# Optimization experiments

Measured on AMD Instinct MI355X. Metric: run time of the kernel, lower is better.

The kernel has to match this reference:

```python
import jax, jax.numpy as jnp
import numpy as np

D_MODEL = 1024
NUM_HEADS = 16
DEPTH = D_MODEL // NUM_HEADS
B, S = 2, 2048


def setup_inputs() -> dict:
    key = jax.random.key(0)
    ks = jax.random.split(key, 8)
    scale = 1.0 / np.sqrt(D_MODEL)
    return {
        "v": jax.random.normal(ks[0], (B, S, D_MODEL), jnp.float32),
        "k": jax.random.normal(ks[1], (B, S, D_MODEL), jnp.float32),
        "q": jax.random.normal(ks[2], (B, S, D_MODEL), jnp.float32),
        "mask": jnp.zeros((B, 1, 1, S), jnp.float32),
        "wq": jax.random.normal(ks[3], (D_MODEL, D_MODEL), jnp.float32) * scale,
        "wk": jax.random.normal(ks[4], (D_MODEL, D_MODEL), jnp.float32) * scale,
        "wv": jax.random.normal(ks[5], (D_MODEL, D_MODEL), jnp.float32) * scale,
        "wo": jax.random.normal(ks[6], (D_MODEL, D_MODEL), jnp.float32) * scale,
        "bq": jnp.zeros((D_MODEL,), jnp.float32),
        "bk": jnp.zeros((D_MODEL,), jnp.float32),
        "bv": jnp.zeros((D_MODEL,), jnp.float32),
        "bo": jnp.zeros((D_MODEL,), jnp.float32),
    }


def _split_heads(x):
    # [B, S, d_model] -> [B, H, S, depth]
    b, s, _ = x.shape
    return x.reshape(b, s, NUM_HEADS, DEPTH).transpose(0, 2, 1, 3)


def reference(v, k, q, mask, wq, wk, wv, wo, bq, bk, bv, bo):
    qh = _split_heads(q @ wq + bq)
    kh = _split_heads(k @ wk + bk)
    vh = _split_heads(v @ wv + bv)
    # scores: [B, H, Sq, Sk]
    scores = jnp.einsum("bhqd,bhkd->bhqk", qh, kh) / jnp.sqrt(
        jnp.asarray(DEPTH, jnp.float32))
    scores = scores + mask * -1e9
    attn = jax.nn.softmax(scores, axis=-1)
    out = jnp.einsum("bhqk,bhkd->bhqd", attn, vh)  # [B, H, Sq, depth]
    out = out.transpose(0, 2, 1, 3).reshape(q.shape[0], -1, D_MODEL)
    out = out @ wo + bo
    return out, attn
```

## Files before the change

kernel.cpp:

```cpp
#include <hip/hip_runtime.h>

#define S_LEN 2048
#define DM 1024
#define NH 16
#define DH 64

typedef __attribute__((ext_vector_type(8))) short short8;
typedef __attribute__((ext_vector_type(4))) float f32x4;
typedef __attribute__((ext_vector_type(16))) float f32x16;
typedef unsigned short u16;
typedef unsigned int u32;

__device__ __forceinline__ u16 f2b(float f){
  union { float f; u32 u; } v; v.f = f;
  return (u16)((v.u + 0x7fffu + ((v.u >> 16) & 1u)) >> 16);
}
__device__ __forceinline__ float b2f(u16 h){
  union { u32 u; float f; } v; v.u = ((u32)h) << 16; return v.f;
}
__device__ __forceinline__ u32 cvtpk(float lo, float hi){
  u32 r;
  asm("v_cvt_pk_bf16_f32 %0, %1, %2" : "=v"(r) : "v"(lo), "v"(hi));
  return r;
}

__device__ __forceinline__ f32x4 mfma16(short8 a, short8 b, f32x4 c){
  return __builtin_amdgcn_mfma_f32_16x16x32_bf16(a, b, c, 0, 0, 0);
}
__device__ __forceinline__ f32x16 mfma32(short8 a, short8 b, f32x16 c){
  return __builtin_amdgcn_mfma_f32_32x32x16_bf16(a, b, c, 0, 0, 0);
}

#define SC2 0.18033688f

#if defined(__has_builtin)
#  if __has_builtin(__builtin_amdgcn_exp2f)
#    define EXP2(x) __builtin_amdgcn_exp2f(x)
#  else
#    define EXP2(x) __expf((x) * 0.6931472f)
#  endif
#else
#  define EXP2(x) __expf((x) * 0.6931472f)
#endif

template<int R, int NT>
__device__ __forceinline__ void stage_tile(const u16* src, int ld, u16* lds){
  const int t = threadIdx.x;
  #pragma unroll
  for (int it = 0; it < R*8/NT; ++it){
    int idx = it*NT + t;
    int row = idx >> 3;
    int ch  = (idx & 7) ^ (row & 7);
    const u16* g = src + row*ld + ch*8;
    u16* l = lds + (it*NT + (t & ~63))*8;
    __builtin_amdgcn_global_load_lds((const __attribute__((address_space(1))) void*)g,
                                     (__attribute__((address_space(3))) void*)l, 16, 0, 0);
  }
}

template<int R, int NT>
__device__ __forceinline__ void stage_tile_f32(const float* src, int ld, u16* lds){
  const int t = threadIdx.x;
  #pragma unroll
  for (int it = 0; it < R*8/NT; ++it){
    int idx = it*NT + t;
    int row = idx >> 3;
    int ch  = (idx & 7) ^ (row & 7);
    const float* g = src + (long)row*ld + ch*8;
    f32x4 a = *(const f32x4*)g;
    f32x4 b = *(const f32x4*)(g + 4);
    union { u32 u[4]; short8 s; } o;
    o.u[0] = cvtpk(a[0], a[1]); o.u[1] = cvtpk(a[2], a[3]);
    o.u[2] = cvtpk(b[0], b[1]); o.u[3] = cvtpk(b[2], b[3]);
    *(short8*)(lds + (long)idx*8) = o.s;
  }
}

__device__ __forceinline__ short8 frag_ld(const u16* tile, int row, int ch){
  int off = (row*128 + ch*16) ^ ((row & 7) << 4);
  return *(const short8*)((const char*)tile + off);
}

__global__ __launch_bounds__(256) void k_pre(
    const float* __restrict__ wq, const float* __restrict__ wk,
    const float* __restrict__ wv, const float* __restrict__ wo,
    u16* __restrict__ oq, u16* __restrict__ ok, u16* __restrict__ ov, u16* __restrict__ oo,
    const float* __restrict__ mask, float* __restrict__ maskb)
{
  __shared__ float tl[64][65];
  const int bid = blockIdx.x, t = threadIdx.x;
  if (bid < 1024){
    int z = bid >> 8, rem = bid & 255;
    const float* W = (z==0)?wq:(z==1)?wk:(z==2)?wv:wo;
    u16* O = (z==0)?oq:(z==1)?ok:(z==2)?ov:oo;
    int k0 = (rem >> 4)*64, n0 = (rem & 15)*64;
    #pragma unroll
    for (int i = 0; i < 16; ++i){
      int idx2 = i*256 + t;
      int row = idx2 >> 6, col = idx2 & 63;
      tl[row][col] = W[(long)(k0+row)*DM + n0 + col];
    }
    __syncthreads();
    #pragma unroll
    for (int i = 0; i < 16; ++i){
      int idx2 = i*256 + t;
      int n = idx2 >> 6, kk = idx2 & 63;
      O[(long)(n0+n)*DM + k0 + kk] = f2b(tl[kk][n]);
    }
  } else {
    int i = (bid - 1024)*256 + t;
    maskb[i] = -1.44269504e9f * mask[i];
  }
}

__device__ __forceinline__ void gemm_body_fused(
    const void* __restrict__ Asrc, const void* __restrict__ Bsrc, int af32,
    const float* __restrict__ bias, u16* __restrict__ dst16,
    int layout, int m0, int n0, u16* At, u16* Bt)
{
  const int t = threadIdx.x, lane = t & 63, w = t >> 6;
  const int wr = (w >> 1) * 64, wc = (w & 1) * 64;
  const int li = lane & 15, lg = lane >> 4;
  const f32x4 zero = {0.f, 0.f, 0.f, 0.f};
  f32x4 acc[4][4];
  #pragma unroll
  for (int m = 0; m < 4; ++m)
    #pragma unroll
    for (int n = 0; n < 4; ++n) acc[m][n] = zero;

  for (int kt = 0; kt < DM/64; ++kt){
    if (af32){
      stage_tile_f32<128,256>((const float*)Asrc + (long)m0*DM + kt*64, DM, At);
      stage_tile<128,256>((const u16*)Bsrc + (long)n0*DM + kt*64, DM, Bt);
    } else {
      stage_tile<128,256>((const u16*)Asrc + (long)m0*DM + kt*64, DM, At);
      stage_tile_f32<128,256>((const float*)Bsrc + (long)n0*DM + kt*64, DM, Bt);
    }
    __syncthreads();
    #pragma unroll
    for (int ks = 0; ks < 2; ++ks){
      int ch = ks*4 + lg;
      short8 a[4], b[4];
      #pragma unroll
      for (int m = 0; m < 4; ++m) a[m] = frag_ld(At, wr + m*16 + li, ch);
      #pragma unroll
      for (int n = 0; n < 4; ++n) b[n] = frag_ld(Bt, wc + n*16 + li, ch);
      #pragma unroll
      for (int m = 0; m < 4; ++m)
        #pragma unroll
        for (int n = 0; n < 4; ++n) acc[m][n] = mfma16(a[m], b[n], acc[m][n]);
    }
    __syncthreads();
  }

  if (layout == 1){
    f32x4 bm[4];
    #pragma unroll
    for (int m = 0; m < 4; ++m) bm[m] = *(const f32x4*)(bias + m0 + wr + m*16 + lg*4);
    #pragma unroll
    for (int m = 0; m < 4; ++m)
      #pragma unroll
      for (int n = 0; n < 4; ++n)
        #pragma unroll
        for (int r = 0; r < 4; ++r){
          int gm = m0 + wr + m*16 + lg*4 + r;
          int gc = n0 + wc + n*16 + li;
          int hh = gm >> 6, dd = gm & 63, bb = gc >> 11, ss = gc & (S_LEN-1);
          dst16[(((long)(bb*NH + hh))*DH + dd)*S_LEN + ss] = f2b(acc[m][n][r] + bm[m][r]);
        }
  } else {
    float bv4[4];
    #pragma unroll
    for (int n = 0; n < 4; ++n) bv4[n] = bias[n0 + wc + n*16 + li];
    #pragma unroll
    for (int m = 0; m < 4; ++m)
      #pragma unroll
      for (int n = 0; n < 4; ++n)
        #pragma unroll
        for (int r = 0; r < 4; ++r){
          int gm = m0 + wr + m*16 + lg*4 + r;
          int gc = n0 + wc + n*16 + li;
          float val = acc[m][n][r] + bv4[n];
          int bb = gm >> 11, ss = gm & (S_LEN-1), hh = gc >> 6, dd = gc & 63;
          dst16[(((long)(bb*NH + hh))*S_LEN + ss)*DH + dd] = f2b(val);
        }
  }
}

__device__ __forceinline__ void gemm_body(const u16* __restrict__ X, const u16* __restrict__ WT,
    const float* __restrict__ bias, float* __restrict__ dst32,
    int m0, int n0, u16* At, u16* Bt)
{
  const int t = threadIdx.x, lane = t & 63, w = t >> 6;
  const int wr = (w >> 1) * 64, wc = (w & 1) * 64;
  const int li = lane & 15, lg = lane >> 4;
  const f32x4 zero = {0.f, 0.f, 0.f, 0.f};
  f32x4 acc[4][4];
  #pragma unroll
  for (int m = 0; m < 4; ++m)
    #pragma unroll
    for (int n = 0; n < 4; ++n) acc[m][n] = zero;

  for (int kt = 0; kt < DM/64; ++kt){
    stage_tile<128,256>(X  + (long)m0*DM + kt*64, DM, At);
    stage_tile<128,256>(WT + (long)n0*DM + kt*64, DM, Bt);
    __syncthreads();
    #pragma unroll
    for (int ks = 0; ks < 2; ++ks){
      int ch = ks*4 + lg;
      short8 a[4], b[4];
      #pragma unroll
      for (int m = 0; m < 4; ++m) a[m] = frag_ld(At, wr + m*16 + li, ch);
      #pragma unroll
      for (int n = 0; n < 4; ++n) b[n] = frag_ld(Bt, wc + n*16 + li, ch);
      #pragma unroll
      for (int m = 0; m < 4; ++m)
        #pragma unroll
        for (int n = 0; n < 4; ++n) acc[m][n] = mfma16(a[m], b[n], acc[m][n]);
    }
    __syncthreads();
  }

  float bv4[4];
  #pragma unroll
  for (int n = 0; n < 4; ++n) bv4[n] = bias[n0 + wc + n*16 + li];
  #pragma unroll
  for (int m = 0; m < 4; ++m)
    #pragma unroll
    for (int n = 0; n < 4; ++n)
      #pragma unroll
      for (int r = 0; r < 4; ++r){
        int gm = m0 + wr + m*16 + lg*4 + r;
        int gc = n0 + wc + n*16 + li;
        dst32[(long)gm*DM + gc] = acc[m][n][r] + bv4[n];
      }
}

__global__ __launch_bounds__(256) void k_gemm_qkv(
    const float* __restrict__ qf, const float* __restrict__ kf, const float* __restrict__ vf,
    const u16* __restrict__ wtq, const u16* __restrict__ wtk, const u16* __restrict__ wtv,
    const float* __restrict__ bq, const float* __restrict__ bk, const float* __restrict__ bv,
    u16* __restrict__ Qw, u16* __restrict__ Kw, u16* __restrict__ VTw)
{
  __shared__ u16 At[128*64], Bt[128*64];
  int bid = blockIdx.x;
  int xcd = bid & 7, j = bid >> 3;
  int z = j >> 5, tt = j & 31;
  int mi = xcd*4 + (tt >> 3), n = tt & 7;
  if (z == 2){
    gemm_body_fused(wtv, vf, 0, bv, VTw, 1, n*128, mi*128, At, Bt);
  } else {
    const float* X = (z==0)?qf:kf;
    const u16* WT  = (z==0)?wtq:wtk;
    const float* B = (z==0)?bq:bk;
    u16* dst = (z==0)?Qw:Kw;
    gemm_body_fused(X, WT, 1, B, dst, 0, mi*128, n*128, At, Bt);
  }
}

__global__ __launch_bounds__(256) void k_gemm_out(
    const u16* __restrict__ ctx, const u16* __restrict__ wto,
    const float* __restrict__ bo, float* __restrict__ out)
{
  __shared__ u16 At[128*64], Bt[128*64];
  int bid = blockIdx.x;
  int xcd = bid & 7, tt = bid >> 3;
  int mi = xcd*4 + (tt >> 3), n = tt & 7;
  gemm_body(ctx, wto, bo, out, mi*128, n*128, At, Bt);
}

__global__ __launch_bounds__(256) void k_attn1(const u16* __restrict__ Q,
    const u16* __restrict__ K, const float* __restrict__ maskb,
    float* __restrict__ lp0, float* __restrict__ lp1)
{
  __shared__ u16 Kt[2][64*64];
  const int t = threadIdx.x, lane = t & 63, w = t >> 6;
  const int lq = lane & 31, hi = lane >> 5;
  const int bid = blockIdx.x;
  const int xcd = bid & 7, j = bid >> 3;
  const int kh = j & 1, jj = j >> 1;
  const int bh = xcd + 8*(jj & 3);
  const int q0 = (jj >> 2) * 128;
  const int b = bh >> 4;
  const int k0 = kh * (S_LEN/2);
  const u16* Qb = Q + ((long)bh*S_LEN + q0 + w*32 + lq)*DH;
  short8 qa[4];
  #pragma unroll
  for (int ds = 0; ds < 4; ++ds) qa[ds] = *(const short8*)(Qb + ds*16 + hi*8);
  const float* mb_g = maskb + b*S_LEN + k0;
  const u16* Kb = K + ((long)bh*S_LEN + k0)*DH;

  float lsum = 0.f;
  stage_tile<64,256>(Kb, DH, Kt[0]);
  __syncthreads();
  for (int tt = 0; tt < S_LEN/128; ++tt){
    const u16* cur = Kt[tt & 1];
    if (tt + 1 < S_LEN/128)
      stage_tile<64,256>(Kb + (long)(tt+1)*64*DH, DH, Kt[(tt+1) & 1]);
    #pragma unroll
    for (int kt = 0; kt < 2; ++kt){
      f32x16 acc = {};
      __builtin_amdgcn_s_setprio(1);
      #pragma unroll
      for (int ds = 0; ds < 4; ++ds)
        acc = mfma32(frag_ld(cur, kt*32 + lq, ds*2 + hi), qa[ds], acc);
      __builtin_amdgcn_s_setprio(0);
      #pragma unroll
      for (int rg = 0; rg < 4; ++rg){
        f32x4 mb = *(const f32x4*)(mb_g + tt*64 + kt*32 + rg*8 + hi*4);
        #pragma unroll
        for (int jj2 = 0; jj2 < 4; ++jj2)
          lsum += EXP2(acc[rg*4+jj2]*SC2 + mb[jj2]);
      }
    }
    __syncthreads();
  }
  lsum += __shfl_xor(lsum, 32);
  if (hi == 0){
    float* lp = kh ? lp1 : lp0;
    lp[bh*S_LEN + q0 + w*32 + lq] = lsum;
  }
}

__global__ __launch_bounds__(256) void k_attn2(const u16* __restrict__ Q,
    const u16* __restrict__ K, const u16* __restrict__ VT,
    const float* __restrict__ maskb, const float* __restrict__ lp0,
    const float* __restrict__ lp1, float* __restrict__ attn, u16* __restrict__ ctx)
{
  __shared__ u16 Kt[2][64*64], Vt[2][64*64], Pt[128*64];
  const int t = threadIdx.x, lane = t & 63, w = t >> 6;
  const int lq = lane & 31, hi = lane >> 5;
  const int bid = blockIdx.x;
  const int xcd = bid & 7, j = bid >> 3;
  const int bh = xcd + 8*(j & 3);
  const int q0 = (j >> 2) * 128;
  const int b = bh >> 4;
  const u16* Qb = Q + ((long)bh*S_LEN + q0 + w*32 + lq)*DH;
  short8 qa[4];
  #pragma unroll
  for (int ds = 0; ds < 4; ++ds) qa[ds] = *(const short8*)(Qb + ds*16 + hi*8);
  const float* mb_g = maskb + b*S_LEN;
  const long lbase = (long)bh*S_LEN + q0 + w*32;

  float rlw[8];
  #pragma unroll
  for (int i = 0; i < 8; ++i){
    int qq = i*4 + (lane >> 4);
    rlw[i] = 1.f / (lp0[lbase + qq] + lp1[lbase + qq]);
  }

  f32x16 cacc[2] = {};
  const int prow = w*32 + lq;
  const int pswz = (prow & 7) << 4;

  stage_tile<64,256>(K  + (long)bh*S_LEN*DH, DH, Kt[0]);
  stage_tile<64,256>(VT + (long)bh*DH*S_LEN, S_LEN, Vt[0]);
  __syncthreads();
  for (int tt = 0; tt < S_LEN/64; ++tt){
    const int cur = tt & 1;
    if (tt + 1 < S_LEN/64){
      stage_tile<64,256>(K  + ((long)bh*S_LEN + (tt+1)*64)*DH, DH, Kt[cur^1]);
      stage_tile<64,256>(VT + (long)bh*DH*S_LEN + (tt+1)*64, S_LEN, Vt[cur^1]);
    }
    #pragma unroll
    for (int kt = 0; kt < 2; ++kt){
      f32x16 acc = {};
      __builtin_amdgcn_s_setprio(1);
      #pragma unroll
      for (int ds = 0; ds < 4; ++ds)
        acc = mfma32(frag_ld(Kt[cur], kt*32 + lq, ds*2 + hi), qa[ds], acc);
      __builtin_amdgcn_s_setprio(0);
      #pragma unroll
      for (int rg = 0; rg < 4; ++rg){
        f32x4 mb = *(const f32x4*)(mb_g + tt*64 + kt*32 + rg*8 + hi*4);
        float p0 = EXP2(acc[rg*4+0]*SC2 + mb[0]);
        float p1 = EXP2(acc[rg*4+1]*SC2 + mb[1]);
        float p2 = EXP2(acc[rg*4+2]*SC2 + mb[2]);
        float p3 = EXP2(acc[rg*4+3]*SC2 + mb[3]);
        uint2 pu;
        pu.x = (u32)f2b(p0) | ((u32)f2b(p1) << 16);
        pu.y = (u32)f2b(p2) | ((u32)f2b(p3) << 16);
        int off = (prow*128 + (kt*32 + rg*8 + hi*4)*2) ^ pswz;
        *(uint2*)((char*)Pt + off) = pu;
      }
    }
    #pragma unroll
    for (int i = 0; i < 8; ++i){
      int rr = i*4 + (lane >> 4);
      int ch8 = lane & 15;
      int roff = ((w*32 + rr)*128 + ch8*8) ^ ((rr & 7) << 4);
      uint2 pr = *(const uint2*)((const char*)Pt + roff);
      f32x4 av;
      av[0] = b2f((u16)(pr.x & 0xffffu)) * rlw[i];
      av[1] = b2f((u16)(pr.x >> 16))     * rlw[i];
      av[2] = b2f((u16)(pr.y & 0xffffu)) * rlw[i];
      av[3] = b2f((u16)(pr.y >> 16))     * rlw[i];
      *(f32x4*)(attn + ((long)bh*S_LEN + q0 + w*32 + rr)*S_LEN + tt*64 + ch8*4) = av;
    }
    short8 pa[4];
    #pragma unroll
    for (int ks = 0; ks < 4; ++ks) pa[ks] = frag_ld(Pt, prow, ks*2 + hi);
    __builtin_amdgcn_s_setprio(1);
    #pragma unroll
    for (int dh = 0; dh < 2; ++dh)
      #pragma unroll
      for (int ks = 0; ks < 4; ++ks)
        cacc[dh] = mfma32(pa[ks], frag_ld(Vt[cur], dh*32 + lq, ks*2 + hi), cacc[dh]);
    __builtin_amdgcn_s_setprio(0);
    asm volatile("s_waitcnt vmcnt(8)" ::: "memory");
    __builtin_amdgcn_sched_barrier(0);
    __builtin_amdgcn_s_barrier();
  }

  int bb = bh >> 4, hh = bh & 15;
  #pragma unroll
  for (int r = 0; r < 16; ++r){
    int qrow = (r & 3) + 8*(r >> 2) + 4*hi;
    float rle = 1.f / (lp0[lbase + qrow] + lp1[lbase + qrow]);
    #pragma unroll
    for (int dh = 0; dh < 2; ++dh){
      float val = cacc[dh][r] * rle;
      ctx[((long)bb*S_LEN + q0 + w*32 + qrow)*DM + hh*DH + dh*32 + lq] = f2b(val);
    }
  }
}

extern "C" void kernel_launch(void* const* d_in, const int* in_sizes, int n_in,
                              void* d_out, int out_size, void* d_ws, size_t ws_size,
                              hipStream_t stream)
{
  const float* v_in = (const float*)d_in[0];
  const float* k_in = (const float*)d_in[1];
  const float* q_in = (const float*)d_in[2];
  const float* mask = (const float*)d_in[3];
  const float* wq = (const float*)d_in[4];
  const float* wk = (const float*)d_in[5];
  const float* wv = (const float*)d_in[6];
  const float* wo = (const float*)d_in[7];
  const float* bq = (const float*)d_in[8];
  const float* bk = (const float*)d_in[9];
  const float* bv = (const float*)d_in[10];
  const float* bo = (const float*)d_in[11];

  float* out  = (float*)d_out;
  float* attn = out + (long)2*S_LEN*DM;

  char* ws = (char*)d_ws;
  const long MW = 1024*1024;
  u16*  wtq = (u16*)(ws);
  u16*  wtk = (u16*)(ws + 2*MW);
  u16*  wtv = (u16*)(ws + 4*MW);
  u16*  wto = (u16*)(ws + 6*MW);
  u16*  Qw  = (u16*)(ws + 35*MW);
  u16*  Kw  = (u16*)(ws + 44*MW);
  u16*  VTw = (u16*)(ws + 53*MW);
  u16*  ctx = (u16*)(ws + 8*MW);
  float* lp0   = (float*)(ws + 62*MW);
  float* lp1   = (float*)(ws + 62*MW + 262144);
  float* maskb = (float*)(ws + 63*MW);

  k_pre<<<1040, 256, 0, stream>>>(wq, wk, wv, wo, wtq, wtk, wtv, wto, mask, maskb);
  k_gemm_qkv<<<768, 256, 0, stream>>>(q_in, k_in, v_in, wtq, wtk, wtv,
                                      bq, bk, bv, Qw, Kw, VTw);
  k_attn1<<<1024, 256, 0, stream>>>(Qw, Kw, maskb, lp0, lp1);
  k_attn2<<<512, 256, 0, stream>>>(Qw, Kw, VTw, maskb, lp0, lp1, attn, ctx);
  k_gemm_out<<<256, 256, 0, stream>>>(ctx, wto, bo, out);
}
```

Baseline: 286.2 us.

## Split attention PV kernel across key halves with fp32 atomic context accumulation

```diff
diff --git a/kernel.cpp b/kernel.cpp
--- a/kernel.cpp
+++ b/kernel.cpp
@@ -185,55 +185,6 @@
           dst16[(((long)(bb*NH + hh))*S_LEN + ss)*DH + dd] = f2b(val);
         }
   }
-}
-
-__device__ __forceinline__ void gemm_body(const u16* __restrict__ X, const u16* __restrict__ WT,
-    const float* __restrict__ bias, float* __restrict__ dst32,
-    int m0, int n0, u16* At, u16* Bt)
-{
-  const int t = threadIdx.x, lane = t & 63, w = t >> 6;
-  const int wr = (w >> 1) * 64, wc = (w & 1) * 64;
-  const int li = lane & 15, lg = lane >> 4;
-  const f32x4 zero = {0.f, 0.f, 0.f, 0.f};
-  f32x4 acc[4][4];
-  #pragma unroll
-  for (int m = 0; m < 4; ++m)
-    #pragma unroll
-    for (int n = 0; n < 4; ++n) acc[m][n] = zero;
-
-  for (int kt = 0; kt < DM/64; ++kt){
-    stage_tile<128,256>(X  + (long)m0*DM + kt*64, DM, At);
-    stage_tile<128,256>(WT + (long)n0*DM + kt*64, DM, Bt);
-    __syncthreads();
-    #pragma unroll
-    for (int ks = 0; ks < 2; ++ks){
-      int ch = ks*4 + lg;
-      short8 a[4], b[4];
-      #pragma unroll
-      for (int m = 0; m < 4; ++m) a[m] = frag_ld(At, wr + m*16 + li, ch);
-      #pragma unroll
-      for (int n = 0; n < 4; ++n) b[n] = frag_ld(Bt, wc + n*16 + li, ch);
-      #pragma unroll
-      for (int m = 0; m < 4; ++m)
-        #pragma unroll
-        for (int n = 0; n < 4; ++n) acc[m][n] = mfma16(a[m], b[n], acc[m][n]);
-    }
-    __syncthreads();
-  }
-
-  float bv4[4];
-  #pragma unroll
-  for (int n = 0; n < 4; ++n) bv4[n] = bias[n0 + wc + n*16 + li];
-  #pragma unroll
-  for (int m = 0; m < 4; ++m)
-    #pragma unroll
-    for (int n = 0; n < 4; ++n)
-      #pragma unroll
-      for (int r = 0; r < 4; ++r){
-        int gm = m0 + wr + m*16 + lg*4 + r;
-        int gc = n0 + wc + n*16 + li;
-        dst32[(long)gm*DM + gc] = acc[m][n][r] + bv4[n];
-      }
 }
 
 __global__ __launch_bounds__(256) void k_gemm_qkv(
@@ -259,14 +210,58 @@
 }
 
 __global__ __launch_bounds__(256) void k_gemm_out(
-    const u16* __restrict__ ctx, const u16* __restrict__ wto,
+    const float* __restrict__ ctx, const u16* __restrict__ wto,
     const float* __restrict__ bo, float* __restrict__ out)
 {
   __shared__ u16 At[128*64], Bt[128*64];
   int bid = blockIdx.x;
   int xcd = bid & 7, tt = bid >> 3;
   int mi = xcd*4 + (tt >> 3), n = tt & 7;
-  gemm_body(ctx, wto, bo, out, mi*128, n*128, At, Bt);
+  int m0 = mi*128, n0 = n*128;
+
+  const int t = threadIdx.x, lane = t & 63, w = t >> 6;
+  const int wr = (w >> 1) * 64, wc = (w & 1) * 64;
+  const int li = lane & 15, lg = lane >> 4;
+  const f32x4 zero = {0.f, 0.f, 0.f, 0.f};
+  f32x4 acc[4][4];
+  #pragma unroll
+  for (int m = 0; m < 4; ++m)
+    #pragma unroll
+    for (int nn = 0; nn < 4; ++nn) acc[m][nn] = zero;
+
+  for (int kt = 0; kt < DM/64; ++kt){
+    stage_tile_f32<128,256>(ctx + (long)m0*DM + kt*64, DM, At);
+    stage_tile<128,256>(wto + (long)n0*DM + kt*64, DM, Bt);
+    __syncthreads();
+    #pragma unroll
+    for (int ks = 0; ks < 2; ++ks){
+      int ch = ks*4 + lg;
+      short8 a[4], b[4];
+      #pragma unroll
+      for (int m = 0; m < 4; ++m) a[m] = frag_ld(At, wr + m*16 + li, ch);
+      #pragma unroll
+      for (int nn = 0; nn < 4; ++nn) b[nn] = frag_ld(Bt, wc + nn*16 + li, ch);
+      #pragma unroll
+      for (int m = 0; m < 4; ++m)
+        #pragma unroll
+        for (int nn = 0; nn < 4; ++nn) acc[m][nn] = mfma16(a[m], b[nn], acc[m][nn]);
+    }
+    __syncthreads();
+  }
+
+  float bv4[4];
+  #pragma unroll
+  for (int nn = 0; nn < 4; ++nn) bv4[nn] = bo[n0 + wc + nn*16 + li];
+  #pragma unroll
+  for (int m = 0; m < 4; ++m)
+    #pragma unroll
+    for (int nn = 0; nn < 4; ++nn)
+      #pragma unroll
+      for (int r = 0; r < 4; ++r){
+        int gm = m0 + wr + m*16 + lg*4 + r;
+        int gc = n0 + wc + nn*16 + li;
+        out[(long)gm*DM + gc] = acc[m][nn][r] + bv4[nn];
+      }
 }
 
 __global__ __launch_bounds__(256) void k_attn1(const u16* __restrict__ Q,
@@ -325,21 +320,25 @@
 __global__ __launch_bounds__(256) void k_attn2(const u16* __restrict__ Q,
     const u16* __restrict__ K, const u16* __restrict__ VT,
     const float* __restrict__ maskb, const float* __restrict__ lp0,
-    const float* __restrict__ lp1, float* __restrict__ attn, u16* __restrict__ ctx)
+    const float* __restrict__ lp1, float* __restrict__ attn, float* __restrict__ ctx)
 {
   __shared__ u16 Kt[2][64*64], Vt[2][64*64], Pt[128*64];
   const int t = threadIdx.x, lane = t & 63, w = t >> 6;
   const int lq = lane & 31, hi = lane >> 5;
   const int bid = blockIdx.x;
   const int xcd = bid & 7, j = bid >> 3;
-  const int bh = xcd + 8*(j & 3);
-  const int q0 = (j >> 2) * 128;
+  const int kh = j & 1, jj = j >> 1;
+  const int bh = xcd + 8*(jj & 3);
+  const int q0 = (jj >> 2) * 128;
   const int b = bh >> 4;
+  const int k0 = kh * (S_LEN/2);
   const u16* Qb = Q + ((long)bh*S_LEN + q0 + w*32 + lq)*DH;
   short8 qa[4];
   #pragma unroll
   for (int ds = 0; ds < 4; ++ds) qa[ds] = *(const short8*)(Qb + ds*16 + hi*8);
-  const float* mb_g = maskb + b*S_LEN;
+  const float* mb_g = maskb + b*S_LEN + k0;
+  const u16* Kb = K  + ((long)bh*S_LEN + k0)*DH;
+  const u16* Vb = VT + (long)bh*DH*S_LEN + k0;
   const long lbase = (long)bh*S_LEN + q0 + w*32;
 
   float rlw[8];
@@ -353,14 +352,14 @@
   const int prow = w*32 + lq;
   const int pswz = (prow & 7) << 4;
 
-  stage_tile<64,256>(K  + (long)bh*S_LEN*DH, DH, Kt[0]);
-  stage_tile<64,256>(VT + (long)bh*DH*S_LEN, S_LEN, Vt[0]);
+  stage_tile<64,256>(Kb, DH, Kt[0]);
+  stage_tile<64,256>(Vb, S_LEN, Vt[0]);
   __syncthreads();
-  for (int tt = 0; tt < S_LEN/64; ++tt){
+  for (int tt = 0; tt < S_LEN/128; ++tt){
     const int cur = tt & 1;
-    if (tt + 1 < S_LEN/64){
-      stage_tile<64,256>(K  + ((long)bh*S_LEN + (tt+1)*64)*DH, DH, Kt[cur^1]);
-      stage_tile<64,256>(VT + (long)bh*DH*S_LEN + (tt+1)*64, S_LEN, Vt[cur^1]);
+    if (tt + 1 < S_LEN/128){
+      stage_tile<64,256>(Kb + (long)(tt+1)*64*DH, DH, Kt[cur^1]);
+      stage_tile<64,256>(Vb + (tt+1)*64, S_LEN, Vt[cur^1]);
     }
     #pragma unroll
     for (int kt = 0; kt < 2; ++kt){
@@ -395,7 +394,7 @@
       av[1] = b2f((u16)(pr.x >> 16))     * rlw[i];
       av[2] = b2f((u16)(pr.y & 0xffffu)) * rlw[i];
       av[3] = b2f((u16)(pr.y >> 16))     * rlw[i];
-      *(f32x4*)(attn + ((long)bh*S_LEN + q0 + w*32 + rr)*S_LEN + tt*64 + ch8*4) = av;
+      *(f32x4*)(attn + ((long)bh*S_LEN + q0 + w*32 + rr)*S_LEN + k0 + tt*64 + ch8*4) = av;
     }
     short8 pa[4];
     #pragma unroll
@@ -420,7 +419,7 @@
     #pragma unroll
     for (int dh = 0; dh < 2; ++dh){
       float val = cacc[dh][r] * rle;
-      ctx[((long)bb*S_LEN + q0 + w*32 + qrow)*DM + hh*DH + dh*32 + lq] = f2b(val);
+      atomicAdd(&ctx[((long)bb*S_LEN + q0 + w*32 + qrow)*DM + hh*DH + dh*32 + lq], val);
     }
   }
 }
@@ -451,18 +450,19 @@
   u16*  wtk = (u16*)(ws + 2*MW);
   u16*  wtv = (u16*)(ws + 4*MW);
   u16*  wto = (u16*)(ws + 6*MW);
+  float* ctx = (float*)(ws + 8*MW);
   u16*  Qw  = (u16*)(ws + 35*MW);
   u16*  Kw  = (u16*)(ws + 44*MW);
   u16*  VTw = (u16*)(ws + 53*MW);
-  u16*  ctx = (u16*)(ws + 8*MW);
   float* lp0   = (float*)(ws + 62*MW);
   float* lp1   = (float*)(ws + 62*MW + 262144);
   float* maskb = (float*)(ws + 63*MW);
 
+  hipMemsetAsync(ctx, 0, (size_t)4096*1024*4, stream);
   k_pre<<<1040, 256, 0, stream>>>(wq, wk, wv, wo, wtq, wtk, wtv, wto, mask, maskb);
   k_gemm_qkv<<<768, 256, 0, stream>>>(q_in, k_in, v_in, wtq, wtk, wtv,
                                       bq, bk, bv, Qw, Kw, VTw);
   k_attn1<<<1024, 256, 0, stream>>>(Qw, Kw, maskb, lp0, lp1);
-  k_attn2<<<512, 256, 0, stream>>>(Qw, Kw, VTw, maskb, lp0, lp1, attn, ctx);
+  k_attn2<<<1024, 256, 0, stream>>>(Qw, Kw, VTw, maskb, lp0, lp1, attn, ctx);
   k_gemm_out<<<256, 256, 0, stream>>>(ctx, wto, bo, out);
 }
```

Measured after the change: 312.1 us. +9.1%, slower.
